# Performance work log

Measured on AMD Instinct MI355X. Metric: run time of the kernel, lower is better.

The kernel has to match this reference:

```python
import jax, jax.numpy as jnp
import numpy as np

B, P, NOBJ = 16, 19248, 32
NUM_CLASSES = 81  # 80 foreground + background (code uses num_classes+1 w/o focal loss)
POS_TH, NEG_TH = 0.5, 0.4
VAR0, VAR1 = 0.1, 0.2  # standard SSD encode variances
NEGPOS_RATIO = 3


def setup_inputs() -> dict:
    key = jax.random.key(0)
    k1, k2, k3, k4, k5 = jax.random.split(key, 5)
    loc_data = jax.random.normal(k1, (B, P, 4), jnp.float32)
    conf_data = jax.random.normal(k2, (B, P, NUM_CLASSES), jnp.float32)
    # priors in (cx, cy, w, h), normalized coords
    pc = jax.random.uniform(k3, (P, 2), jnp.float32, 0.05, 0.95)
    pw = jax.random.uniform(jax.random.fold_in(k3, 1), (P, 2), jnp.float32, 0.05, 0.4)
    priors = jnp.concatenate([pc, pw], -1)
    # gt boxes in point form (xmin, ymin, xmax, ymax)
    gc = jax.random.uniform(k4, (B, NOBJ, 2), jnp.float32, 0.2, 0.8)
    gw = jax.random.uniform(jax.random.fold_in(k4, 1), (B, NOBJ, 2), jnp.float32, 0.05, 0.3)
    gt_boxes = jnp.concatenate([gc - gw / 2, gc + gw / 2], -1)
    gt_labels = jax.random.randint(k5, (B, NOBJ), 0, NUM_CLASSES - 1)  # 0..79
    return {"loc_data": loc_data, "conf_data": conf_data, "priors": priors,
            "gt_boxes": gt_boxes, "gt_labels": gt_labels}


def _point_form(p):
    # (cx,cy,w,h) -> (xmin,ymin,xmax,ymax)
    return jnp.concatenate([p[..., :2] - p[..., 2:] / 2, p[..., :2] + p[..., 2:] / 2], -1)


def _jaccard(a, b):
    # a: [N,4], b: [P,4] point form -> IoU [N,P]
    lt = jnp.maximum(a[:, None, :2], b[None, :, :2])
    rb = jnp.minimum(a[:, None, 2:], b[None, :, 2:])
    wh = jnp.clip(rb - lt, 0.0)
    inter = wh[..., 0] * wh[..., 1]
    area_a = (a[:, 2] - a[:, 0]) * (a[:, 3] - a[:, 1])
    area_b = (b[:, 2] - b[:, 0]) * (b[:, 3] - b[:, 1])
    return inter / (area_a[:, None] + area_b[None, :] - inter)


def _match_one(gt, labels, priors_pf, priors):
    # SSD match: per-prior best gt + force each gt's best prior to be positive
    ov = _jaccard(gt, priors_pf)                 # [N,P]
    best_prior_idx = jnp.argmax(ov, axis=1)      # [N]
    best_truth_ov = jnp.max(ov, axis=0)          # [P]
    best_truth_idx = jnp.argmax(ov, axis=0)      # [P]
    best_truth_ov = best_truth_ov.at[best_prior_idx].set(2.0)
    best_truth_idx = best_truth_idx.at[best_prior_idx].set(jnp.arange(gt.shape[0]))
    matched = gt[best_truth_idx]                 # [P,4] point form
    conf = labels[best_truth_idx] + 1
    conf = jnp.where(best_truth_ov < POS_TH, -1, conf)   # neutral band
    conf = jnp.where(best_truth_ov < NEG_TH, 0, conf)    # background
    # encode offsets with variances
    m_cxcy = (matched[:, :2] + matched[:, 2:]) / 2
    m_wh = matched[:, 2:] - matched[:, :2]
    g_cxcy = (m_cxcy - priors[:, :2]) / (VAR0 * priors[:, 2:])
    g_wh = jnp.log(m_wh / priors[:, 2:]) / VAR1
    return jnp.concatenate([g_cxcy, g_wh], -1), conf


def reference(loc_data, conf_data, priors, gt_boxes, gt_labels):
    priors_pf = _point_form(priors)
    loc_t, conf_t = jax.vmap(lambda g, l: _match_one(g, l, priors_pf, priors))(gt_boxes, gt_labels)
    loc_t = jax.lax.stop_gradient(loc_t)
    pos = conf_t > 0                                   # [B,P]
    n_pos = pos.sum(axis=1)                            # [B]
    N = jnp.maximum(pos.sum(), 1).astype(loc_data.dtype)
    # localization: smooth L1 over positives
    d = loc_data - loc_t
    ad = jnp.abs(d)
    sl1 = jnp.where(ad < 1.0, 0.5 * d * d, ad - 0.5)
    loss_l = jnp.sum(sl1 * pos[..., None])
    # confidence: hard negative mining at 3:1
    logp = jax.nn.log_softmax(conf_data, axis=-1)      # [B,P,C]
    ct = jnp.maximum(conf_t, 0)
    nll = -jnp.take_along_axis(logp, ct[..., None], axis=-1)[..., 0]  # [B,P]
    mine = jnp.where(pos | (conf_t < 0), 0.0, nll)     # exclude pos & neutral from mining
    rank = jnp.argsort(jnp.argsort(-mine, axis=1), axis=1)
    num_neg = jnp.minimum(NEGPOS_RATIO * n_pos, P - 1)
    neg = (rank < num_neg[:, None]) & (conf_t == 0)
    loss_c = jnp.sum(nll * (pos | neg))
    return jnp.stack([loss_l, loss_c]) / N
```

## Files before the change

### kernel.cpp

```cpp
#include <hip/hip_runtime.h>
#include <cstdint>
#include <cstddef>

#define BB 16
#define PP 19248
#define NOBJ 32
#define NCLS 81
#define POS_TH 0.5f
#define NEG_TH 0.4f
#define VAR0 0.1f
#define VAR1 0.2f
#define NEGPOS 3

#define MTB 256
#define NMB ((PP + MTB - 1) / MTB)
#define MAINB 1024
#define ROWS_PB 64
#define NSLOT ((PP + ROWS_PB - 1) / ROWS_PB)
#define ST 1024

#define HSHIFT 19
#define HSIZE 8192
#define HPT (HSIZE / ST)
#define CAP HSIZE

__global__ __launch_bounds__(MTB) void k_match(const float* __restrict__ priors,
                                               const float* __restrict__ gt_boxes,
                                               unsigned long long* __restrict__ gkey) {
    const int b = blockIdx.y;
    const int p = blockIdx.x * MTB + threadIdx.x;
    const int wid = threadIdx.x >> 6, lane = threadIdx.x & 63;
    __shared__ float4 sg[NOBJ];
    __shared__ unsigned long long wkey[4][NOBJ];
    if (threadIdx.x < NOBJ) sg[threadIdx.x] = ((const float4*)gt_boxes)[b * NOBJ + threadIdx.x];
    __syncthreads();

    const bool valid = p < PP;
    float px1 = 0.f, py1 = 0.f, px2 = 0.f, py2 = 0.f, parea = 0.f;
    if (valid) {
        float4 pr = ((const float4*)priors)[p];
        float hw = pr.z / 2.0f, hh = pr.w / 2.0f;
        px1 = pr.x - hw; py1 = pr.y - hh; px2 = pr.x + hw; py2 = pr.y + hh;
        parea = (px2 - px1) * (py2 - py1);
    }

    for (int n = 0; n < NOBJ; ++n) {
        float4 g = sg[n];
        float iou = -1.0f;
        if (valid) {
            {
#pragma clang fp contract(off)
                float ix1 = fmaxf(g.x, px1), iy1 = fmaxf(g.y, py1);
                float ix2 = fminf(g.z, px2), iy2 = fminf(g.w, py2);
                float iw = fmaxf(ix2 - ix1, 0.0f), ih = fmaxf(iy2 - iy1, 0.0f);
                float inter = iw * ih;
                float garea = (g.z - g.x) * (g.w - g.y);
                iou = inter / (garea + parea - inter);
            }
        }

        float m = iou;
        m = fmaxf(m, __shfl_xor(m, 1, 64));
        m = fmaxf(m, __shfl_xor(m, 2, 64));
        m = fmaxf(m, __shfl_xor(m, 4, 64));
        m = fmaxf(m, __shfl_xor(m, 8, 64));
        m = fmaxf(m, __shfl_xor(m, 16, 64));
        m = fmaxf(m, __shfl_xor(m, 32, 64));
        unsigned long long ball = __ballot(iou == m);
        if (lane == 0) {
            unsigned long long key = 0ull;
            if (m >= 0.0f) {
                unsigned psrc = (unsigned)(blockIdx.x * MTB + wid * 64 +
                                           (int)__builtin_ctzll(ball));
                key = (((unsigned long long)__float_as_uint(m)) << 32) |
                      (unsigned long long)(0xFFFFFFFFu - psrc);
            }
            wkey[wid][n] = key;
        }
    }

    __syncthreads();
    if (threadIdx.x < NOBJ) {
        unsigned long long k0 = wkey[0][threadIdx.x];
        unsigned long long k1 = wkey[1][threadIdx.x];
        unsigned long long k2 = wkey[2][threadIdx.x];
        unsigned long long k3 = wkey[3][threadIdx.x];
        if (k1 > k0) k0 = k1;
        if (k2 > k0) k0 = k2;
        if (k3 > k0) k0 = k3;
        atomicMax(&gkey[b * NOBJ + threadIdx.x], k0);
    }
}

__device__ __forceinline__ float sl1(float d) {
    float ad = fabsf(d);
    return ad < 1.0f ? 0.5f * d * d : ad - 0.5f;
}

__global__ __launch_bounds__(MAINB, 8) void k_main(const float* __restrict__ loc_data,
                                                   const float* __restrict__ conf_data,
                                                   const float* __restrict__ priors,
                                                   const float* __restrict__ gt_boxes,
                                                   const int* __restrict__ gt_labels,
                                                   const unsigned long long* __restrict__ gkey,
                                                   float* __restrict__ mine,
                                                   float* __restrict__ p_ll,
                                                   float* __restrict__ p_lc,
                                                   int* __restrict__ p_np) {
    const int b = blockIdx.y;
    const int t = threadIdx.x;
    const int wid = t >> 6;
    const int lane = t & 63;
    const int g = lane >> 4;
    const int j = lane & 15;
    const int rbase = blockIdx.x * ROWS_PB + wid * 4;
    const int r = rbase + g;
    const bool valid = r < PP;

    unsigned pst = 0xFFFFFFFFu;
    if (lane < NOBJ) {
        unsigned long long key = gkey[b * NOBJ + lane];
        pst = 0xFFFFFFFFu - (unsigned)(key & 0xFFFFFFFFull);
    }

    const float* rowp = conf_data + ((size_t)b * PP + r) * NCLS;
    float c0 = 0.f, c1 = 0.f, c2 = 0.f, c3 = 0.f, c4 = 0.f, c80 = 0.f;
    float4 pr = make_float4(0.f, 0.f, 0.f, 0.f);
    if (valid) {
        c0 = rowp[j];
        c1 = rowp[j + 16];
        c2 = rowp[j + 32];
        c3 = rowp[j + 48];
        c4 = rowp[j + 64];
        if (j == 0) c80 = rowp[80];
        pr = ((const float4*)priors)[r];
    }
    float4 ga = ((const float4*)gt_boxes)[b * NOBJ + j];
    float4 gb = ((const float4*)gt_boxes)[b * NOBJ + j + 16];
    float bov;
    int bidx;
    {
#pragma clang fp contract(off)
        float hw = pr.z / 2.0f, hh = pr.w / 2.0f;
        float px1 = pr.x - hw, py1 = pr.y - hh, px2 = pr.x + hw, py2 = pr.y + hh;
        float parea = (px2 - px1) * (py2 - py1);

        float ix1 = fmaxf(ga.x, px1), iy1 = fmaxf(ga.y, py1);
        float ix2 = fminf(ga.z, px2), iy2 = fminf(ga.w, py2);
        float iw = fmaxf(ix2 - ix1, 0.0f), ih = fmaxf(iy2 - iy1, 0.0f);
        float inter = iw * ih;
        float garea = (ga.z - ga.x) * (ga.w - ga.y);
        float iouA = inter / (garea + parea - inter);

        ix1 = fmaxf(gb.x, px1); iy1 = fmaxf(gb.y, py1);
        ix2 = fminf(gb.z, px2); iy2 = fminf(gb.w, py2);
        iw = fmaxf(ix2 - ix1, 0.0f); ih = fmaxf(iy2 - iy1, 0.0f);
        inter = iw * ih;
        garea = (gb.z - gb.x) * (gb.w - gb.y);
        float iouB = inter / (garea + parea - inter);

        bov = iouA; bidx = j;
        if (iouB > bov) { bov = iouB; bidx = j + 16; }
    }
#pragma unroll
    for (int m = 1; m < 16; m <<= 1) {
        float o = __shfl_xor(bov, m, 64);
        int oi = __shfl_xor(bidx, m, 64);
        if (o > bov || (o == bov && oi < bidx)) { bov = o; bidx = oi; }
    }

    float s = __expf(c0) + __expf(c1) + __expf(c2) + __expf(c3) + __expf(c4);
    if (j == 0) s += __expf(c80);
    s += __shfl_xor(s, 1, 64);
    s += __shfl_xor(s, 2, 64);
    s += __shfl_xor(s, 4, 64);
    s += __shfl_xor(s, 8, 64);
    const float lse = __logf(s);

    unsigned long long b0 = __ballot(pst == (unsigned)(rbase + 0));
    unsigned long long b1 = __ballot(pst == (unsigned)(rbase + 1));
    unsigned long long b2 = __ballot(pst == (unsigned)(rbase + 2));
    unsigned long long b3 = __ballot(pst == (unsigned)(rbase + 3));
    unsigned long long mball = (g == 0) ? b0 : (g == 1) ? b1 : (g == 2) ? b2 : b3;

    float my_ll = 0.0f, my_lc = 0.0f;
    int my_pos = 0;

    if (valid && j == 0) {
        const size_t idx = (size_t)b * PP + r;
        float ov = bov;
        int ti = bidx;
        if (mball) { ov = 2.0f; ti = 63 - __builtin_clzll(mball); }
        int conf_c = gt_labels[b * NOBJ + ti] + 1;
        if (ov < POS_TH) conf_c = -1;
        if (ov < NEG_TH) conf_c = 0;
        const int ct = conf_c > 0 ? conf_c : 0;
        const float nll = lse - rowp[ct];

        if (conf_c > 0) {
            my_pos = 1;
            my_lc = nll;
            float4 gbox = ((const float4*)gt_boxes)[b * NOBJ + ti];
            float mcx = (gbox.x + gbox.z) / 2.0f, mcy = (gbox.y + gbox.w) / 2.0f;
            float mw = gbox.z - gbox.x, mh = gbox.w - gbox.y;
            float t0 = (mcx - pr.x) / (VAR0 * pr.z);
            float t1 = (mcy - pr.y) / (VAR0 * pr.w);
            float t2 = logf(mw / pr.z) / VAR1;
            float t3 = logf(mh / pr.w) / VAR1;
            float4 ld = ((const float4*)loc_data)[(size_t)b * PP + r];
            my_ll = sl1(ld.x - t0) + sl1(ld.y - t1) + sl1(ld.z - t2) + sl1(ld.w - t3);
        }
        mine[idx] = (conf_c == 0) ? nll : 0.0f;
    }

    for (int off = 32; off > 0; off >>= 1) {
        my_ll += __shfl_down(my_ll, off, 64);
        my_lc += __shfl_down(my_lc, off, 64);
        my_pos += __shfl_down(my_pos, off, 64);
    }
    __shared__ float rll[16], rlc[16];
    __shared__ int rnp[16];
    if (lane == 0) { rll[wid] = my_ll; rlc[wid] = my_lc; rnp[wid] = my_pos; }
    __syncthreads();
    if (t == 0) {
        float a = 0.0f, c = 0.0f;
        int n = 0;
#pragma unroll
        for (int w = 0; w < 16; ++w) { a += rll[w]; c += rlc[w]; n += rnp[w]; }
        p_ll[b * NSLOT + blockIdx.x] = a;
        p_lc[b * NSLOT + blockIdx.x] = c;
        p_np[b * NSLOT + blockIdx.x] = n;
    }
}

__global__ __launch_bounds__(ST) void k_select(const float* __restrict__ mine,
                                               const float* __restrict__ p_ll,
                                               const float* __restrict__ p_lc,
                                               const int* __restrict__ p_np,
                                               float* __restrict__ acc,
                                               int* __restrict__ acc_np,
                                               unsigned* __restrict__ done,
                                               float* __restrict__ out) {
    const int b = blockIdx.x;
    const int tid = threadIdx.x;
    const int wid = tid >> 6, lane = tid & 63;
    constexpr int NW = ST / 64;

    __shared__ unsigned hist[HSIZE];
    __shared__ unsigned s_tsum[ST];
    __shared__ unsigned s_wsum[NW];
    __shared__ float rll[NW], rlc[NW];
    __shared__ int rnp[NW];
    __shared__ float rs1[NW], rs2[NW];
    __shared__ unsigned rc2[NW];
    __shared__ float s_ll, s_lc, s_neg;
    __shared__ int s_np, s_B, s_G1;
    __shared__ unsigned s_cntB, s_cnt, s_prefix;
    __shared__ int s_rem;
    __shared__ unsigned h16[16];
    __shared__ unsigned swh[NW * 16];
    __shared__ unsigned stot[16];

    float ll = 0.0f, lc = 0.0f;
    int np = 0;
    for (int i = tid; i < NSLOT; i += ST) {
        ll += p_ll[b * NSLOT + i];
        lc += p_lc[b * NSLOT + i];
        np += p_np[b * NSLOT + i];
    }
    for (int off = 32; off > 0; off >>= 1) {
        ll += __shfl_down(ll, off, 64);
        lc += __shfl_down(lc, off, 64);
        np += __shfl_down(np, off, 64);
    }
    if (lane == 0) { rll[wid] = ll; rlc[wid] = lc; rnp[wid] = np; }
    __syncthreads();
    if (tid == 0) {
        float a = 0.0f, c = 0.0f;
        int n = 0;
        for (int w = 0; w < NW; ++w) { a += rll[w]; c += rlc[w]; n += rnp[w]; }
        s_ll = a; s_lc = c; s_np = n;
        s_neg = 0.0f;
    }
    __syncthreads();
    const int np_b = s_np;
    const int k = min(NEGPOS * np_b, PP - 1);

    const float* mv = mine + (size_t)b * PP;
    const float4* mv4 = (const float4*)mv;
    constexpr int PP4 = PP / 4;

    if (k > 0) {
        for (int i = tid; i < HSIZE; i += ST) hist[i] = 0u;
        __syncthreads();
        for (int i = tid; i < PP4; i += ST) {
            float4 v = mv4[i];
            atomicAdd(&hist[__float_as_uint(v.x) >> HSHIFT], 1u);
            atomicAdd(&hist[__float_as_uint(v.y) >> HSHIFT], 1u);
            atomicAdd(&hist[__float_as_uint(v.z) >> HSHIFT], 1u);
            atomicAdd(&hist[__float_as_uint(v.w) >> HSHIFT], 1u);
        }
        __syncthreads();

        unsigned tsum = 0;
        const int hb = tid * HPT;
#pragma unroll
        for (int v = 0; v < HPT; ++v) tsum += hist[hb + v];
        s_tsum[tid] = tsum;
        unsigned wsum = tsum;
        for (int off = 32; off > 0; off >>= 1) wsum += __shfl_down(wsum, off, 64);
        if (lane == 0) s_wsum[wid] = wsum;
        __syncthreads();
        if (tid == 0) {
            unsigned cum = 0;
            int w = NW - 1;
            for (; w > 0; --w) {
                if (cum + s_wsum[w] >= (unsigned)k) break;
                cum += s_wsum[w];
            }
            int t = (w + 1) * 64 - 1;
            for (; t > w * 64; --t) {
                if (cum + s_tsum[t] >= (unsigned)k) break;
                cum += s_tsum[t];
            }
            int bin = t * HPT + HPT - 1;
            for (; bin > t * HPT; --bin) {
                if (cum + hist[bin] >= (unsigned)k) break;
                cum += hist[bin];
            }
            s_B = bin;
            s_G1 = (int)cum;
            s_cntB = hist[bin];
            s_cnt = 0u;
        }
        __syncthreads();
        const int B = s_B;
        const int r = k - s_G1;
        const unsigned cntB = s_cntB;
        const unsigned bin_lo = (unsigned)B << HSHIFT;
        const unsigned hi_base = (unsigned)(B + 1) << HSHIFT;
        unsigned* cbuf = hist;

        if (cntB <= CAP) {
            float S1 = 0.0f;
            for (int i = tid; i < PP4; i += ST) {
                float4 v = mv4[i];
                unsigned bx = __float_as_uint(v.x);
                unsigned by = __float_as_uint(v.y);
                unsigned bz = __float_as_uint(v.z);
                unsigned bw = __float_as_uint(v.w);
                if (bx >= hi_base) S1 += v.x;
                else if (bx >= bin_lo) cbuf[atomicAdd(&s_cnt, 1u)] = bx;
                if (by >= hi_base) S1 += v.y;
                else if (by >= bin_lo) cbuf[atomicAdd(&s_cnt, 1u)] = by;
                if (bz >= hi_base) S1 += v.z;
                else if (bz >= bin_lo) cbuf[atomicAdd(&s_cnt, 1u)] = bz;
                if (bw >= hi_base) S1 += v.w;
                else if (bw >= bin_lo) cbuf[atomicAdd(&s_cnt, 1u)] = bw;
            }
            for (int off = 32; off > 0; off >>= 1) S1 += __shfl_down(S1, off, 64);
            if (lane == 0) rs1[wid] = S1;
            __syncthreads();

            if (tid == 0) { s_prefix = bin_lo; s_rem = r; }
            __syncthreads();
            for (int pass = 0; pass < 5; ++pass) {
                const int shift = (pass < 4) ? (15 - 4 * pass) : 0;
                const int width = (pass < 4) ? 4 : 3;
                const int nb = 1 << width;
                const unsigned hm = 0xFFFFFFFFu << (shift + width);
                if (tid < 16) h16[tid] = 0u;
                __syncthreads();
                const unsigned prefix = s_prefix;
                for (unsigned i = tid; i < cntB; i += ST) {
                    unsigned bits = cbuf[i];
                    if ((bits & hm) == prefix)
                        atomicAdd(&h16[(bits >> shift) & (nb - 1)], 1u);
                }
                __syncthreads();
                if (tid == 0) {
                    int rem = s_rem;
                    unsigned cum = 0;
                    int chosen = 0;
                    for (int v = nb - 1; v >= 0; --v) {
                        unsigned c = h16[v];
                        if (cum + c >= (unsigned)rem) { chosen = v; s_rem = rem - (int)cum; break; }
                        cum += c;
                    }
                    s_prefix = prefix | ((unsigned)chosen << shift);
                }
                __syncthreads();
            }
            const unsigned T = s_prefix;

            float S2 = 0.0f;
            unsigned c2 = 0;
            for (unsigned i = tid; i < cntB; i += ST) {
                unsigned bits = cbuf[i];
                if (bits > T) { S2 += __uint_as_float(bits); c2++; }
            }
            for (int off = 32; off > 0; off >>= 1) {
                S2 += __shfl_down(S2, off, 64);
                c2 += __shfl_down(c2, off, 64);
            }
            if (lane == 0) { rs2[wid] = S2; rc2[wid] = c2; }
            __syncthreads();
            if (tid == 0) {
                float S1t = 0.0f, S2t = 0.0f;
                unsigned c2t = 0;
                for (int w = 0; w < NW; ++w) { S1t += rs1[w]; S2t += rs2[w]; c2t += rc2[w]; }
                s_neg = S1t + S2t + (float)(r - (int)c2t) * __uint_as_float(T);
            }
            __syncthreads();
        } else {
            if (tid == 0) { s_prefix = 0u; s_rem = k; }
            __syncthreads();
            for (int pass = 0; pass < 8; ++pass) {
                const int shift = 28 - 4 * pass;
                const unsigned hm = (pass == 0) ? 0u : (0xFFFFFFFFu << (shift + 4));
                const unsigned prefix = s_prefix;
                unsigned cnt[16];
#pragma unroll
                for (int v = 0; v < 16; ++v) cnt[v] = 0u;
                for (int i = tid; i < PP; i += ST) {
                    unsigned bits = __float_as_uint(mv[i]);
                    unsigned key = ((bits & hm) == prefix) ? ((bits >> shift) & 15u) : 16u;
                    if (__any(key != 16u)) {
#pragma unroll
                        for (int v = 0; v < 16; ++v)
                            cnt[v] += (unsigned)__popcll(__ballot(key == (unsigned)v));
                    }
                }
                if (lane == 0) {
#pragma unroll
                    for (int v = 0; v < 16; ++v) swh[wid * 16 + v] = cnt[v];
                }
                __syncthreads();
                if (tid < 16) {
                    unsigned tt = 0;
#pragma unroll
                    for (int w = 0; w < NW; ++w) tt += swh[w * 16 + tid];
                    stot[tid] = tt;
                }
                __syncthreads();
                if (tid == 0) {
                    int rem = s_rem;
                    unsigned cum = 0;
                    int chosen = 0;
                    for (int v = 15; v >= 0; --v) {
                        unsigned c = stot[v];
                        if (cum + c >= (unsigned)rem) { chosen = v; s_rem = rem - (int)cum; break; }
                        cum += c;
                    }
                    s_prefix = prefix | ((unsigned)chosen << shift);
                }
                __syncthreads();
            }
            const unsigned T = s_prefix;
            float sum = 0.0f;
            unsigned cnt = 0;
            for (int i = tid; i < PP; i += ST) {
                float v = mv[i];
                if (__float_as_uint(v) > T) { sum += v; cnt++; }
            }
            for (int off = 32; off > 0; off >>= 1) {
                sum += __shfl_down(sum, off, 64);
                cnt += __shfl_down(cnt, off, 64);
            }
            if (lane == 0) { rs2[wid] = sum; rc2[wid] = cnt; }
            __syncthreads();
            if (tid == 0) {
                float S = 0.0f;
                int G = 0;
                for (int w = 0; w < NW; ++w) { S += rs2[w]; G += (int)rc2[w]; }
                s_neg = S + (float)(k - G) * __uint_as_float(T);
            }
            __syncthreads();
        }
    }

    if (tid == 0) {
        atomicAdd(&acc[0], s_ll);
        atomicAdd(&acc[1], s_lc + s_neg);
        atomicAdd(acc_np, np_b);
        __threadfence();
        unsigned prev = atomicAdd(done, 1u);
        if (prev == BB - 1) {
            int tp = atomicAdd(acc_np, 0);
            float N = (float)max(tp, 1);
            float a0 = atomicAdd(&acc[0], 0.0f);
            float a1 = atomicAdd(&acc[1], 0.0f);
            out[0] = a0 / N;
            out[1] = a1 / N;
        }
    }
}

extern "C" void kernel_launch(void* const* d_in, const int* in_sizes, int n_in,
                              void* d_out, int out_size, void* d_ws, size_t ws_size,
                              hipStream_t stream) {
    const float* loc    = (const float*)d_in[0];
    const float* conf   = (const float*)d_in[1];
    const float* priors = (const float*)d_in[2];
    const float* gt     = (const float*)d_in[3];
    const int*   labels = (const int*)d_in[4];
    float* out = (float*)d_out;

    char* ws = (char*)d_ws;
    const size_t SZ_BP = (size_t)BB * PP * 4;
    const size_t SZ_SLOT = (size_t)BB * NSLOT * 4;
    unsigned long long* gkey = (unsigned long long*)ws;
    float*    acc    = (float*)   (ws + 4096);
    int*      acc_np = (int*)     (ws + 4104);
    unsigned* done   = (unsigned*)(ws + 4108);
    float* mine = (float*)(ws + 4224);
    float* p_ll = (float*)(ws + 4224 + SZ_BP);
    float* p_lc = (float*)(ws + 4224 + SZ_BP + SZ_SLOT);
    int*   p_np = (int*)  (ws + 4224 + SZ_BP + 2 * SZ_SLOT);

    (void)hipMemsetAsync(ws, 0, 4224, stream);

    dim3 mg(NMB, BB);
    k_match<<<mg, MTB, 0, stream>>>(priors, gt, gkey);

    dim3 kg(NSLOT, BB);
    k_main<<<kg, MAINB, 0, stream>>>(loc, conf, priors, gt, labels, gkey,
                                     mine, p_ll, p_lc, p_np);

    k_select<<<BB, ST, 0, stream>>>(mine, p_ll, p_lc, p_np, acc, acc_np, done, out);
}
```

Before: 217.2 us.

## Split matching into per-gt chunked argmax and per-prior best-gt kernels

The match kernel now assigns each wavefront a (batch, gt, prior-chunk) job and does one packed-key argmax with a single atomic, replacing the per-gt wave reductions and ballots. A new k_prior kernel computes each prior's best gt and its pos/neutral/neg class once and writes them packed into a workspace buffer. k_main reads that buffer instead of recomputing IoU with shuffles, and writes per-wave partial sums without a block-level reduction and syncthreads. This adds an extra kernel launch and an extra B×P int buffer write/read in exchange for less redundant IoU and reduction work in the main kernel.

```diff
diff --git a/kernel.cpp b/kernel.cpp
--- a/kernel.cpp
+++ b/kernel.cpp
@@ -17,7 +17,13 @@
 #define MAINB 1024
 #define ROWS_PB 64
 #define NSLOT ((PP + ROWS_PB - 1) / ROWS_PB)
+#define NSLOTW (NSLOT * 16)
 #define ST 1024
+
+#define MCH 8
+#define CHLEN (PP / MCH)
+#define MJOBS (BB * NOBJ * MCH)
+#define MBLK (MJOBS / 4)
 
 #define HSHIFT 19
 #define HSIZE 8192
@@ -27,69 +33,88 @@
 __global__ __launch_bounds__(MTB) void k_match(const float* __restrict__ priors,
                                                const float* __restrict__ gt_boxes,
                                                unsigned long long* __restrict__ gkey) {
+    const int wid = threadIdx.x >> 6, lane = threadIdx.x & 63;
+    const int job = blockIdx.x * 4 + wid;
+    const int b = job >> 8;
+    const int n = (job >> 3) & 31;
+    const int c = job & 7;
+
+    const float4 g = ((const float4*)gt_boxes)[b * NOBJ + n];
+    float garea;
+    {
+#pragma clang fp contract(off)
+        garea = (g.z - g.x) * (g.w - g.y);
+    }
+
+    unsigned long long bestkey = 0ull;
+    const int pbeg = c * CHLEN;
+    const int pend = pbeg + CHLEN;
+    for (int p = pbeg + lane; p < pend; p += 64) {
+        float4 pr = ((const float4*)priors)[p];
+        float iou;
+        {
+#pragma clang fp contract(off)
+            float hw = pr.z / 2.0f, hh = pr.w / 2.0f;
+            float px1 = pr.x - hw, py1 = pr.y - hh, px2 = pr.x + hw, py2 = pr.y + hh;
+            float parea = (px2 - px1) * (py2 - py1);
+            float ix1 = fmaxf(g.x, px1), iy1 = fmaxf(g.y, py1);
+            float ix2 = fminf(g.z, px2), iy2 = fminf(g.w, py2);
+            float iw = fmaxf(ix2 - ix1, 0.0f), ih = fmaxf(iy2 - iy1, 0.0f);
+            float inter = iw * ih;
+            iou = inter / (garea + parea - inter);
+        }
+        unsigned long long key = (((unsigned long long)__float_as_uint(iou)) << 32) |
+                                 (unsigned long long)(0xFFFFFFFFu - (unsigned)p);
+        if (key > bestkey) bestkey = key;
+    }
+#pragma unroll
+    for (int m = 1; m < 64; m <<= 1) {
+        unsigned long long o = __shfl_xor(bestkey, m, 64);
+        if (o > bestkey) bestkey = o;
+    }
+    if (lane == 0) atomicMax(&gkey[b * NOBJ + n], bestkey);
+}
+
+__global__ __launch_bounds__(MTB) void k_prior(const float* __restrict__ priors,
+                                               const float* __restrict__ gt_boxes,
+                                               int* __restrict__ bp) {
     const int b = blockIdx.y;
     const int p = blockIdx.x * MTB + threadIdx.x;
-    const int wid = threadIdx.x >> 6, lane = threadIdx.x & 63;
     __shared__ float4 sg[NOBJ];
-    __shared__ unsigned long long wkey[4][NOBJ];
     if (threadIdx.x < NOBJ) sg[threadIdx.x] = ((const float4*)gt_boxes)[b * NOBJ + threadIdx.x];
     __syncthreads();
-
-    const bool valid = p < PP;
-    float px1 = 0.f, py1 = 0.f, px2 = 0.f, py2 = 0.f, parea = 0.f;
-    if (valid) {
-        float4 pr = ((const float4*)priors)[p];
+    if (p >= PP) return;
+
+    float4 pr = ((const float4*)priors)[p];
+    float px1, py1, px2, py2, parea;
+    {
+#pragma clang fp contract(off)
         float hw = pr.z / 2.0f, hh = pr.w / 2.0f;
         px1 = pr.x - hw; py1 = pr.y - hh; px2 = pr.x + hw; py2 = pr.y + hh;
         parea = (px2 - px1) * (py2 - py1);
     }
 
+    float best = -1.0f;
+    int bn = 0;
+#pragma unroll 4
     for (int n = 0; n < NOBJ; ++n) {
         float4 g = sg[n];
-        float iou = -1.0f;
-        if (valid) {
-            {
+        float iou;
+        {
 #pragma clang fp contract(off)
-                float ix1 = fmaxf(g.x, px1), iy1 = fmaxf(g.y, py1);
-                float ix2 = fminf(g.z, px2), iy2 = fminf(g.w, py2);
-                float iw = fmaxf(ix2 - ix1, 0.0f), ih = fmaxf(iy2 - iy1, 0.0f);
-                float inter = iw * ih;
-                float garea = (g.z - g.x) * (g.w - g.y);
-                iou = inter / (garea + parea - inter);
-            }
-        }
-
-        float m = iou;
-        m = fmaxf(m, __shfl_xor(m, 1, 64));
-        m = fmaxf(m, __shfl_xor(m, 2, 64));
-        m = fmaxf(m, __shfl_xor(m, 4, 64));
-        m = fmaxf(m, __shfl_xor(m, 8, 64));
-        m = fmaxf(m, __shfl_xor(m, 16, 64));
-        m = fmaxf(m, __shfl_xor(m, 32, 64));
-        unsigned long long ball = __ballot(iou == m);
-        if (lane == 0) {
-            unsigned long long key = 0ull;
-            if (m >= 0.0f) {
-                unsigned psrc = (unsigned)(blockIdx.x * MTB + wid * 64 +
-                                           (int)__builtin_ctzll(ball));
-                key = (((unsigned long long)__float_as_uint(m)) << 32) |
-                      (unsigned long long)(0xFFFFFFFFu - psrc);
-            }
-            wkey[wid][n] = key;
-        }
-    }
-
-    __syncthreads();
-    if (threadIdx.x < NOBJ) {
-        unsigned long long k0 = wkey[0][threadIdx.x];
-        unsigned long long k1 = wkey[1][threadIdx.x];
-        unsigned long long k2 = wkey[2][threadIdx.x];
-        unsigned long long k3 = wkey[3][threadIdx.x];
-        if (k1 > k0) k0 = k1;
-        if (k2 > k0) k0 = k2;
-        if (k3 > k0) k0 = k3;
-        atomicMax(&gkey[b * NOBJ + threadIdx.x], k0);
-    }
+            float ix1 = fmaxf(g.x, px1), iy1 = fmaxf(g.y, py1);
+            float ix2 = fminf(g.z, px2), iy2 = fminf(g.w, py2);
+            float iw = fmaxf(ix2 - ix1, 0.0f), ih = fmaxf(iy2 - iy1, 0.0f);
+            float inter = iw * ih;
+            float garea = (g.z - g.x) * (g.w - g.y);
+            iou = inter / (garea + parea - inter);
+        }
+        if (iou > best) { best = iou; bn = n; }
+    }
+    int cls = 2;
+    if (best < POS_TH) cls = 1;
+    if (best < NEG_TH) cls = 0;
+    bp[(size_t)b * PP + p] = (bn << 2) | cls;
 }
 
 __device__ __forceinline__ float sl1(float d) {
@@ -97,16 +122,17 @@
     return ad < 1.0f ? 0.5f * d * d : ad - 0.5f;
 }
 
-__global__ __launch_bounds__(MAINB, 8) void k_main(const float* __restrict__ loc_data,
-                                                   const float* __restrict__ conf_data,
-                                                   const float* __restrict__ priors,
-                                                   const float* __restrict__ gt_boxes,
-                                                   const int* __restrict__ gt_labels,
-                                                   const unsigned long long* __restrict__ gkey,
-                                                   float* __restrict__ mine,
-                                                   float* __restrict__ p_ll,
-                                                   float* __restrict__ p_lc,
-                                                   int* __restrict__ p_np) {
+__global__ __launch_bounds__(MAINB) void k_main(const float* __restrict__ loc_data,
+                                                const float* __restrict__ conf_data,
+                                                const float* __restrict__ priors,
+                                                const float* __restrict__ gt_boxes,
+                                                const int* __restrict__ gt_labels,
+                                                const int* __restrict__ bp,
+                                                const unsigned long long* __restrict__ gkey,
+                                                float* __restrict__ mine,
+                                                float* __restrict__ p_ll,
+                                                float* __restrict__ p_lc,
+                                                int* __restrict__ p_np) {
     const int b = blockIdx.y;
     const int t = threadIdx.x;
     const int wid = t >> 6;
@@ -116,16 +142,18 @@
     const int rbase = blockIdx.x * ROWS_PB + wid * 4;
     const int r = rbase + g;
     const bool valid = r < PP;
+    const int slot = blockIdx.x * 16 + wid;
 
     unsigned pst = 0xFFFFFFFFu;
+    int labreg = 0;
     if (lane < NOBJ) {
-        unsigned long long key = gkey[b * NOBJ + lane];
-        pst = 0xFFFFFFFFu - (unsigned)(key & 0xFFFFFFFFull);
+        pst = 0xFFFFFFFFu - (unsigned)(gkey[b * NOBJ + lane] & 0xFFFFFFFFull);
+        labreg = gt_labels[b * NOBJ + lane];
     }
 
     const float* rowp = conf_data + ((size_t)b * PP + r) * NCLS;
     float c0 = 0.f, c1 = 0.f, c2 = 0.f, c3 = 0.f, c4 = 0.f, c80 = 0.f;
-    float4 pr = make_float4(0.f, 0.f, 0.f, 0.f);
+    int packed = 0;
     if (valid) {
         c0 = rowp[j];
         c1 = rowp[j + 16];
@@ -133,40 +161,7 @@
         c3 = rowp[j + 48];
         c4 = rowp[j + 64];
         if (j == 0) c80 = rowp[80];
-        pr = ((const float4*)priors)[r];
-    }
-    float4 ga = ((const float4*)gt_boxes)[b * NOBJ + j];
-    float4 gb = ((const float4*)gt_boxes)[b * NOBJ + j + 16];
-    float bov;
-    int bidx;
-    {
-#pragma clang fp contract(off)
-        float hw = pr.z / 2.0f, hh = pr.w / 2.0f;
-        float px1 = pr.x - hw, py1 = pr.y - hh, px2 = pr.x + hw, py2 = pr.y + hh;
-        float parea = (px2 - px1) * (py2 - py1);
-
-        float ix1 = fmaxf(ga.x, px1), iy1 = fmaxf(ga.y, py1);
-        float ix2 = fminf(ga.z, px2), iy2 = fminf(ga.w, py2);
-        float iw = fmaxf(ix2 - ix1, 0.0f), ih = fmaxf(iy2 - iy1, 0.0f);
-        float inter = iw * ih;
-        float garea = (ga.z - ga.x) * (ga.w - ga.y);
-        float iouA = inter / (garea + parea - inter);
-
-        ix1 = fmaxf(gb.x, px1); iy1 = fmaxf(gb.y, py1);
-        ix2 = fminf(gb.z, px2); iy2 = fminf(gb.w, py2);
-        iw = fmaxf(ix2 - ix1, 0.0f); ih = fmaxf(iy2 - iy1, 0.0f);
-        inter = iw * ih;
-        garea = (gb.z - gb.x) * (gb.w - gb.y);
-        float iouB = inter / (garea + parea - inter);
-
-        bov = iouA; bidx = j;
-        if (iouB > bov) { bov = iouB; bidx = j + 16; }
-    }
-#pragma unroll
-    for (int m = 1; m < 16; m <<= 1) {
-        float o = __shfl_xor(bov, m, 64);
-        int oi = __shfl_xor(bidx, m, 64);
-        if (o > bov || (o == bov && oi < bidx)) { bov = o; bidx = oi; }
+        packed = bp[(size_t)b * PP + r];
     }
 
     float s = __expf(c0) + __expf(c1) + __expf(c2) + __expf(c3) + __expf(c4);
@@ -183,24 +178,26 @@
     unsigned long long b3 = __ballot(pst == (unsigned)(rbase + 3));
     unsigned long long mball = (g == 0) ? b0 : (g == 1) ? b1 : (g == 2) ? b2 : b3;
 
+    int ti = packed >> 2;
+    int cls = packed & 3;
+    if (mball) { ti = 63 - __builtin_clzll(mball); cls = 2; }
+
+    const int lab = __shfl(labreg, ti, 64);
+    int conf_c = (cls == 2) ? (lab + 1) : ((cls == 1) ? -1 : 0);
+
+    const float row0 = __shfl(c0, lane & 48, 64);
+    const float nll0 = lse - row0;
+
     float my_ll = 0.0f, my_lc = 0.0f;
     int my_pos = 0;
 
     if (valid && j == 0) {
-        const size_t idx = (size_t)b * PP + r;
-        float ov = bov;
-        int ti = bidx;
-        if (mball) { ov = 2.0f; ti = 63 - __builtin_clzll(mball); }
-        int conf_c = gt_labels[b * NOBJ + ti] + 1;
-        if (ov < POS_TH) conf_c = -1;
-        if (ov < NEG_TH) conf_c = 0;
-        const int ct = conf_c > 0 ? conf_c : 0;
-        const float nll = lse - rowp[ct];
-
+        mine[(size_t)b * PP + r] = (conf_c == 0) ? nll0 : 0.0f;
         if (conf_c > 0) {
             my_pos = 1;
-            my_lc = nll;
+            my_lc = lse - rowp[conf_c];
             float4 gbox = ((const float4*)gt_boxes)[b * NOBJ + ti];
+            float4 pr = ((const float4*)priors)[r];
             float mcx = (gbox.x + gbox.z) / 2.0f, mcy = (gbox.y + gbox.w) / 2.0f;
             float mw = gbox.z - gbox.x, mh = gbox.w - gbox.y;
             float t0 = (mcx - pr.x) / (VAR0 * pr.z);
@@ -210,26 +207,25 @@
             float4 ld = ((const float4*)loc_data)[(size_t)b * PP + r];
             my_ll = sl1(ld.x - t0) + sl1(ld.y - t1) + sl1(ld.z - t2) + sl1(ld.w - t3);
         }
-        mine[idx] = (conf_c == 0) ? nll : 0.0f;
-    }
-
-    for (int off = 32; off > 0; off >>= 1) {
-        my_ll += __shfl_down(my_ll, off, 64);
-        my_lc += __shfl_down(my_lc, off, 64);
-        my_pos += __shfl_down(my_pos, off, 64);
-    }
-    __shared__ float rll[16], rlc[16];
-    __shared__ int rnp[16];
-    if (lane == 0) { rll[wid] = my_ll; rlc[wid] = my_lc; rnp[wid] = my_pos; }
-    __syncthreads();
-    if (t == 0) {
-        float a = 0.0f, c = 0.0f;
-        int n = 0;
-#pragma unroll
-        for (int w = 0; w < 16; ++w) { a += rll[w]; c += rlc[w]; n += rnp[w]; }
-        p_ll[b * NSLOT + blockIdx.x] = a;
-        p_lc[b * NSLOT + blockIdx.x] = c;
-        p_np[b * NSLOT + blockIdx.x] = n;
+    }
+
+    if (__ballot(my_pos != 0) == 0ull) {
+        if (lane == 0) {
+            p_ll[b * NSLOTW + slot] = 0.0f;
+            p_lc[b * NSLOTW + slot] = 0.0f;
+            p_np[b * NSLOTW + slot] = 0;
+        }
+    } else {
+        for (int off = 32; off > 0; off >>= 1) {
+            my_ll += __shfl_down(my_ll, off, 64);
+            my_lc += __shfl_down(my_lc, off, 64);
+            my_pos += __shfl_down(my_pos, off, 64);
+        }
+        if (lane == 0) {
+            p_ll[b * NSLOTW + slot] = my_ll;
+            p_lc[b * NSLOTW + slot] = my_lc;
+            p_np[b * NSLOTW + slot] = my_pos;
+        }
     }
 }
 
@@ -263,10 +259,10 @@
 
     float ll = 0.0f, lc = 0.0f;
     int np = 0;
-    for (int i = tid; i < NSLOT; i += ST) {
-        ll += p_ll[b * NSLOT + i];
-        lc += p_lc[b * NSLOT + i];
-        np += p_np[b * NSLOT + i];
+    for (int i = tid; i < NSLOTW; i += ST) {
+        ll += p_ll[b * NSLOTW + i];
+        lc += p_lc[b * NSLOTW + i];
+        np += p_np[b * NSLOTW + i];
     }
     for (int off = 32; off > 0; off >>= 1) {
         ll += __shfl_down(ll, off, 64);
@@ -508,23 +504,26 @@
 
     char* ws = (char*)d_ws;
     const size_t SZ_BP = (size_t)BB * PP * 4;
-    const size_t SZ_SLOT = (size_t)BB * NSLOT * 4;
+    const size_t SZ_SLOT = (size_t)BB * NSLOTW * 4;
     unsigned long long* gkey = (unsigned long long*)ws;
     float*    acc    = (float*)   (ws + 4096);
     int*      acc_np = (int*)     (ws + 4104);
     unsigned* done   = (unsigned*)(ws + 4108);
-    float* mine = (float*)(ws + 4224);
-    float* p_ll = (float*)(ws + 4224 + SZ_BP);
-    float* p_lc = (float*)(ws + 4224 + SZ_BP + SZ_SLOT);
-    int*   p_np = (int*)  (ws + 4224 + SZ_BP + 2 * SZ_SLOT);
+    int*   bp   = (int*)  (ws + 4224);
+    float* mine = (float*)(ws + 4224 + SZ_BP);
+    float* p_ll = (float*)(ws + 4224 + 2 * SZ_BP);
+    float* p_lc = (float*)(ws + 4224 + 2 * SZ_BP + SZ_SLOT);
+    int*   p_np = (int*)  (ws + 4224 + 2 * SZ_BP + 2 * SZ_SLOT);
 
     (void)hipMemsetAsync(ws, 0, 4224, stream);
 
-    dim3 mg(NMB, BB);
-    k_match<<<mg, MTB, 0, stream>>>(priors, gt, gkey);
+    k_match<<<MBLK, MTB, 0, stream>>>(priors, gt, gkey);
+
+    dim3 pg(NMB, BB);
+    k_prior<<<pg, MTB, 0, stream>>>(priors, gt, bp);
 
     dim3 kg(NSLOT, BB);
-    k_main<<<kg, MAINB, 0, stream>>>(loc, conf, priors, gt, labels, gkey,
+    k_main<<<kg, MAINB, 0, stream>>>(loc, conf, priors, gt, labels, bp, gkey,
                                      mine, p_ll, p_lc, p_np);
 
     k_select<<<BB, ST, 0, stream>>>(mine, p_ll, p_lc, p_np, acc, acc_np, done, out);
```

Measured after the change: 213.6 us. Within noise of the previous version (-1.7%).
